# Kernel optimization log

Hardware: AMD Instinct MI355X
Metric: run time of the kernel (lower is better)

Reference implementation:

```python
import jax, jax.numpy as jnp
from jax import lax
import numpy as np

RF = 1024   # receptive field
MGC = 60    # mgc feature size
UPS = 200   # upsample factor
MIX = 10    # num mixtures
FS = 256    # filter size
F = 2       # mgc frames
N = F * UPS
SQRT_HALF = 0.70710678118


def setup_inputs() -> dict:
    key = jax.random.key(0)
    ks = jax.random.split(key, 30)
    g = lambda i, shape, s=0.05: jax.random.normal(ks[i], shape, dtype=jnp.float32) * s
    return dict(
        signal=g(0, (N + RF,), 0.3),
        mgc=g(1, (F, MGC), 1.0),
        cond_w=g(2, (MGC * UPS, MGC)), cond_b=g(3, (MGC * UPS,)),
        l0_win=g(4, (FS, 1, 2)), l0_bin=g(5, (FS,)),
        l0_wg=g(6, (FS, 1, 2)), l0_bg=g(7, (FS,)),
        l0_wr=g(8, (FS, 1, 2)), l0_br=g(9, (FS,)),
        lw_in=g(10, (9, FS, FS, 2)), lb_in=g(11, (9, FS)),
        lw_g=g(12, (9, FS, FS, 2)), lb_g=g(13, (9, FS)),
        lw_r=g(14, (9, FS, FS, 2)), lb_r=g(15, (9, FS)),
        cw_in=g(16, (10, FS, MGC)), cb_in=g(17, (10, FS)),
        cw_g=g(18, (10, FS, MGC)), cb_g=g(19, (10, FS)),
        pre_w=g(20, (256, FS)), pre_b=g(21, (256,)),
        mean_w=g(22, (MIX, 256)), mean_b=g(23, (MIX,)),
        std_w=g(24, (MIX, 256)), std_b=g(25, (MIX,)),
        logit_w=g(26, (MIX, 256)), logit_b=g(27, (MIX,)),
    )


def _cond_conv(x, cond, win, bin_, wg, bg, wr, br, wci, bci, wcg, bcg):
    # x: [N, Cin, L]; cond: [N, MGC] -> out: [N, FS, L//2]
    conv = lambda w, b: lax.conv_general_dilated(
        x, w, window_strides=(2,), padding='VALID',
        dimension_numbers=('NCH', 'OIH', 'NCH')) + b[None, :, None]
    it = jnp.tanh(conv(win, bin_) + (cond @ wci.T + bci)[:, :, None])
    gt = jax.nn.sigmoid(conv(wg, bg) + (cond @ wcg.T + bcg)[:, :, None])
    return (it * gt + conv(wr, br)) * SQRT_HALF


def _forward(signal, mgc, cond_w, cond_b,
             l0_win, l0_bin, l0_wg, l0_bg, l0_wr, l0_br,
             lw_in, lb_in, lw_g, lb_g, lw_r, lb_r,
             cw_in, cb_in, cw_g, cb_g,
             pre_w, pre_b, mean_w, mean_b, std_w, std_b, logit_w, logit_b):
    n = signal.shape[0] - RF
    # sliding windows: [n, 1, RF]
    idx = jnp.arange(n)[:, None] + jnp.arange(RF)[None, :]
    x = signal[idx][:, None, :]
    # conditioning: [F, MGC] -> [F, MGC*UPS] -> [F*UPS, MGC]
    cond = jnp.tanh(mgc @ cond_w.T + cond_b).reshape(-1, MGC)
    # WaveNet stack: 10 stride-2 gated conv layers, L: 1024 -> 1
    x = _cond_conv(x, cond, l0_win, l0_bin, l0_wg, l0_bg, l0_wr, l0_br,
                   cw_in[0], cb_in[0], cw_g[0], cb_g[0])
    for i in range(9):
        x = _cond_conv(x, cond, lw_in[i], lb_in[i], lw_g[i], lb_g[i],
                       lw_r[i], lb_r[i], cw_in[i + 1], cb_in[i + 1],
                       cw_g[i + 1], cb_g[i + 1])
    pre = jax.nn.relu(x[:, :, 0] @ pre_w.T + pre_b)  # [n, 256]
    mean = pre @ mean_w.T + mean_b
    stdev = pre @ std_w.T + std_b
    logits = pre @ logit_w.T + logit_b
    return mean, stdev, logits


def reference(signal, mgc, cond_w, cond_b,
              l0_win, l0_bin, l0_wg, l0_bg, l0_wr, l0_br,
              lw_in, lb_in, lw_g, lb_g, lw_r, lb_r,
              cw_in, cb_in, cw_g, cb_g,
              pre_w, pre_b, mean_w, mean_b, std_w, std_b, logit_w, logit_b):
    return _forward(signal, mgc, cond_w, cond_b,
                    l0_win, l0_bin, l0_wg, l0_bg, l0_wr, l0_br,
                    lw_in, lb_in, lw_g, lb_g, lw_r, lb_r,
                    cw_in, cb_in, cw_g, cb_g,
                    pre_w, pre_b, mean_w, mean_b, std_w, std_b,
                    logit_w, logit_b)
```

## Files before the change

kernel.cpp:

```cpp
#include <hip/hip_runtime.h>

typedef unsigned short u16;
using bf16x8 = __attribute__((ext_vector_type(8))) short;
using f32x4  = __attribute__((ext_vector_type(4))) float;

#define SQRT_HALF 0.70710678118f

__device__ __forceinline__ u16 f2bf(float f) {
    union { float f; unsigned int i; } x; x.f = f;
    unsigned int i = x.i;
    unsigned int r = (i + 0x7FFFu + ((i >> 16) & 1u)) >> 16;
    return (u16)r;
}
__device__ __forceinline__ float bf2f(u16 u) {
    union { unsigned int i; float f; } x; x.i = ((unsigned int)u) << 16; return x.f;
}
__device__ __forceinline__ float fastrcp(float x) {
    float r; asm("v_rcp_f32 %0, %1" : "=v"(r) : "v"(x)); return r;
}
__device__ __forceinline__ float sigm(float x) {
    return fastrcp(1.0f + __expf(-x));
}
__device__ __forceinline__ float tanh_f(float x) {
    float cx = fminf(fmaxf(x, -12.f), 12.f);
    float e = __expf(2.f * cx);
    return 1.0f - 2.0f * fastrcp(e + 1.0f);
}

__device__ __forceinline__ void gld16(const u16* g, u16* l) {
    __builtin_amdgcn_global_load_lds(
        (const __attribute__((address_space(1))) void*)g,
        (__attribute__((address_space(3))) void*)l,
        16, 0, 0);
}

__global__ __launch_bounds__(256) void xpose_kernel(
        const float* __restrict__ cond_w, const float* __restrict__ cw_in,
        const float* __restrict__ cw_g,
        float* __restrict__ cond_wT, float* __restrict__ cwT_in,
        float* __restrict__ cwT_g) {
    int idx = blockIdx.x * 256 + threadIdx.x;
    if (idx < 720000) {
        int c = idx / 12000, j = idx % 12000;
        cond_wT[idx] = cond_w[(size_t)j * 60 + c];
    } else if (idx < 720000 + 153600) {
        int i = idx - 720000;
        int l = i / 15360, r = i % 15360;
        int cc = r / 256, co = r % 256;
        cwT_in[i] = cw_in[((size_t)(l * 256 + co)) * 60 + cc];
    } else if (idx < 720000 + 307200) {
        int i = idx - 720000 - 153600;
        int l = i / 15360, r = i % 15360;
        int cc = r / 256, co = r % 256;
        cwT_g[i] = cw_g[((size_t)(l * 256 + co)) * 60 + cc];
    }
}

__global__ __launch_bounds__(256) void prep_kernel(
        const float* __restrict__ mgc, const float* __restrict__ cond_wT,
        const float* __restrict__ cond_b,
        const float* __restrict__ cwT_in, const float* __restrict__ cb_in,
        const float* __restrict__ cwT_g,  const float* __restrict__ cb_g,
        const float* __restrict__ l0_bin, const float* __restrict__ lb_in,
        const float* __restrict__ l0_bg,  const float* __restrict__ lb_g,
        const float* __restrict__ lw_in, const float* __restrict__ lw_g,
        const float* __restrict__ lw_r,
        float* __restrict__ ca_in, float* __restrict__ ca_g,
        u16* __restrict__ Wg, u16* __restrict__ Wt) {
    int b = blockIdx.x, t = threadIdx.x;
    if (b < 500) {
        __shared__ float c2[8][60];
        int l = b / 50, ng = b % 50;
        int n0 = ng * 8;
        int f = n0 / 200;
        for (int e = t; e < 480; e += 256) {
            int dn = e / 60, cc = e % 60;
            int jj = ((n0 + dn) % 200) * 60 + cc;
            float s = cond_b[jj];
            const float* mrow = mgc + f * 60;
            for (int c = 0; c < 60; ++c) s += mrow[c] * cond_wT[c * 12000 + jj];
            c2[dn][cc] = tanh_f(s);
        }
        __syncthreads();
        int co = t;
        float sib = cb_in[l * 256 + co] + (l == 0 ? l0_bin[co] : lb_in[(l - 1) * 256 + co]);
        float sgb = cb_g [l * 256 + co] + (l == 0 ? l0_bg [co] : lb_g [(l - 1) * 256 + co]);
        float si[8], sg[8];
        #pragma unroll
        for (int dn = 0; dn < 8; ++dn) { si[dn] = sib; sg[dn] = sgb; }
        const float* wiT = cwT_in + l * 15360 + co;
        const float* wgT = cwT_g  + l * 15360 + co;
        for (int cc = 0; cc < 60; ++cc) {
            float wiv = wiT[cc * 256];
            float wgv = wgT[cc * 256];
            #pragma unroll
            for (int dn = 0; dn < 8; ++dn) {
                float cv = c2[dn][cc];
                si[dn] += cv * wiv;
                sg[dn] += cv * wgv;
            }
        }
        #pragma unroll
        for (int dn = 0; dn < 8; ++dn) {
            ca_in[l * 102400 + (n0 + dn) * 256 + co] = si[dn];
            ca_g [l * 102400 + (n0 + dn) * 256 + co] = sg[dn];
        }
    } else if (b < 5108) {
        int idx = (b - 500) * 256 + t;
        if (idx < 9 * 256 * 512) {
            int kk = idx & 511;
            int co = (idx >> 9) & 255;
            int l  = idx >> 17;
            int k = kk >> 8, ci = kk & 255;
            size_t src = ((size_t)(l * 256 + co) * 256 + ci) * 2 + k;
            size_t dst = (size_t)l * 3 * 131072 + (size_t)co * 512 + kk;
            Wg[dst]              = f2bf(lw_in[src]);
            Wg[dst + 131072]     = f2bf(lw_g[src]);
            Wg[dst + 2 * 131072] = f2bf(lw_r[src]);
        }
    } else {
        int c = (b - 5108) * 256 + t;
        if (c < 245760) {
            int lane = c & 63;
            int t1 = c >> 6;
            int cf = t1 & 7;
            int t2 = t1 >> 3;
            int kk = t2 & 15;
            int t3 = t2 >> 4;
            int cb = t3 & 1;
            int t4 = t3 >> 1;
            int cv = t4 % 3;
            int l5 = t4 / 3;
            int q = lane >> 4, r16 = lane & 15;
            int co = cb * 128 + cf * 16 + r16;
            const float* w = cv == 0 ? lw_in : (cv == 1 ? lw_g : lw_r);
            u16* dst = Wt + (size_t)c * 8;
            #pragma unroll
            for (int j = 0; j < 8; ++j) {
                int kdim = kk * 32 + q * 8 + j;
                int tap = kdim >> 8, ci = kdim & 255;
                size_t src = (((size_t)((l5 + 4) * 256 + co)) * 256 + ci) * 2 + tap;
                dst[j] = f2bf(w[src]);
            }
        }
    }
}

__global__ void l0_kernel(const float* __restrict__ signal,
                          const float* __restrict__ l0_win, const float* __restrict__ l0_wg,
                          const float* __restrict__ l0_wr,  const float* __restrict__ l0_br,
                          const float* __restrict__ ca_in0, const float* __restrict__ ca_g0,
                          u16* __restrict__ Y0, int n_start) {
    int b = blockIdx.x;
    int tg = b & 127, n_local = b >> 7;
    int n = n_start + n_local;
    int ci = threadIdx.x;
    float wi0 = l0_win[ci * 2], wi1 = l0_win[ci * 2 + 1];
    float wg0 = l0_wg [ci * 2], wg1 = l0_wg [ci * 2 + 1];
    float wr0 = l0_wr [ci * 2], wr1 = l0_wr [ci * 2 + 1];
    float cain = ca_in0[n * 256 + ci], cag = ca_g0[n * 256 + ci], br = l0_br[ci];
    for (int i = 0; i < 4; ++i) {
        int t = tg * 4 + i;
        float s0 = signal[n + 2 * t];
        float s1 = signal[n + 2 * t + 1];
        float vin = wi0 * s0 + wi1 * s1 + cain;
        float vg  = wg0 * s0 + wg1 * s1 + cag;
        float vr  = wr0 * s0 + wr1 * s1 + br;
        float o = (tanh_f(vin) * sigm(vg) + vr) * SQRT_HALF;
        Y0[((size_t)n_local * 512 + t) * 256 + ci] = f2bf(o);
    }
}

template<int BK>
__global__ __launch_bounds__(256, BK == 32 ? 3 : 2) void gemm_layer_kernel(
        const u16* __restrict__ A, const u16* __restrict__ Wg,
        const float* __restrict__ ca_in, const float* __restrict__ ca_g,
        const float* __restrict__ br, u16* __restrict__ Y,
        int M, int lg, int n_start) {
    constexpr int AC  = BK / 16;
    constexpr int BC  = (3 * BK) / 32;
    constexpr int SL  = BK / 8;
    constexpr int RSH = (BK == 32) ? 2 : 3;
    constexpr int NS  = 512 / BK;

    __shared__ __attribute__((aligned(16))) u16 A0[128 * BK];
    __shared__ __attribute__((aligned(16))) u16 A1[128 * BK];
    __shared__ __attribute__((aligned(16))) u16 B0[192 * BK];
    __shared__ __attribute__((aligned(16))) u16 B1[192 * BK];

    int mtiles = (M + 127) >> 7;
    int b = blockIdx.x;
    int mtile, cotile;
    if ((mtiles & 7) == 0) {
        int g = b >> 5, r = b & 31;
        mtile  = g * 8 + (r & 7);
        cotile = r >> 3;
    } else {
        mtile = b >> 2; cotile = b & 3;
    }
    int m0  = mtile * 128;
    int co0 = cotile * 64;
    int tid = threadIdx.x;
    int lane = tid & 63, wave = tid >> 6;
    int wm = wave & 1, wc = wave >> 1;
    int q = lane >> 4, r16 = lane & 15;

    auto swz = [](int row) { return (BK == 32) ? ((row >> 1) & 3) : (row & 7); };

    const u16* agp[AC]; unsigned aoff[AC];
    #pragma unroll
    for (int i = 0; i < AC; ++i) {
        int c = i * 256 + tid;
        int row = c >> RSH, s = c & (SL - 1);
        int m = m0 + row;
        int msafe = m < M ? m : (M - 1);
        agp[i] = A + (size_t)msafe * 512 + (s ^ swz(row)) * 8;
        aoff[i] = (unsigned)c * 8;
    }
    const u16* bgp[BC]; unsigned boff[BC];
    #pragma unroll
    for (int i = 0; i < BC; ++i) {
        int c = i * 256 + tid;
        int row = c >> RSH, s = c & (SL - 1);
        int conv = row >> 6, col = row & 63;
        bgp[i] = Wg + ((size_t)conv * 256 + co0 + col) * 512 + (s ^ swz(row)) * 8;
        boff[i] = (unsigned)c * 8;
    }

    f32x4 acc[3][4][2] = {};

    auto doIssue = [&](int ktn, u16* Al, u16* Bl) {
        #pragma unroll
        for (int i = 0; i < AC; ++i) gld16(agp[i] + ktn * BK, &Al[aoff[i]]);
        #pragma unroll
        for (int i = 0; i < BC; ++i) gld16(bgp[i] + ktn * BK, &Bl[boff[i]]);
    };
    auto doComp = [&](const u16* Al, const u16* Bl) {
        #pragma unroll
        for (int ks = 0; ks < BK / 32; ++ks) {
            bf16x8 af[4], bfr[3][2];
            #pragma unroll
            for (int ms = 0; ms < 4; ++ms) {
                int row = wm * 64 + ms * 16 + r16;
                af[ms] = *(const bf16x8*)(&Al[row * BK + (((ks * 4 + q) ^ swz(row)) * 8)]);
            }
            #pragma unroll
            for (int cv = 0; cv < 3; ++cv)
                #pragma unroll
                for (int cs = 0; cs < 2; ++cs) {
                    int row = cv * 64 + wc * 32 + cs * 16 + r16;
                    bfr[cv][cs] = *(const bf16x8*)(&Bl[row * BK + (((ks * 4 + q) ^ swz(row)) * 8)]);
                }
            __builtin_amdgcn_s_setprio(1);
            #pragma unroll
            for (int cv = 0; cv < 3; ++cv)
                #pragma unroll
                for (int ms = 0; ms < 4; ++ms)
                    #pragma unroll
                    for (int cs = 0; cs < 2; ++cs)
                        acc[cv][ms][cs] = __builtin_amdgcn_mfma_f32_16x16x32_bf16(
                            af[ms], bfr[cv][cs], acc[cv][ms][cs], 0, 0, 0);
            __builtin_amdgcn_s_setprio(0);
        }
    };
    auto waitv = []() {
        if constexpr (BK == 32)
            asm volatile("s_waitcnt vmcnt(5)\n\ts_barrier" ::: "memory");
        else
            asm volatile("s_waitcnt vmcnt(10)\n\ts_barrier" ::: "memory");
    };

    doIssue(0, A0, B0);
    doIssue(1, A1, B1);
    waitv();

    #pragma unroll
    for (int kt2 = 0; kt2 < NS / 2 - 1; ++kt2) {
        doComp(A0, B0);
        asm volatile("s_waitcnt lgkmcnt(0)\n\ts_barrier" ::: "memory");
        doIssue(2 * kt2 + 2, A0, B0);
        waitv();
        doComp(A1, B1);
        asm volatile("s_waitcnt lgkmcnt(0)\n\ts_barrier" ::: "memory");
        doIssue(2 * kt2 + 3, A1, B1);
        waitv();
    }
    doComp(A0, B0);
    asm volatile("s_waitcnt lgkmcnt(0)\n\ts_barrier" ::: "memory");
    asm volatile("s_waitcnt vmcnt(0)\n\ts_barrier" ::: "memory");
    doComp(A1, B1);

    #pragma unroll
    for (int ms = 0; ms < 4; ++ms) {
        #pragma unroll
        for (int reg = 0; reg < 4; ++reg) {
            int m = m0 + wm * 64 + ms * 16 + q * 4 + reg;
            if (m >= M) continue;
            int n = n_start + (m >> lg);
            #pragma unroll
            for (int cs = 0; cs < 2; ++cs) {
                int co = co0 + wc * 32 + cs * 16 + r16;
                float vin = acc[0][ms][cs][reg] + ca_in[n * 256 + co];
                float vg  = acc[1][ms][cs][reg] + ca_g [n * 256 + co];
                float vr  = acc[2][ms][cs][reg] + br[co];
                float o = (tanh_f(vin) * sigm(vg) + vr) * SQRT_HALF;
                Y[(size_t)m * 256 + co] = f2bf(o);
            }
        }
    }
}

__global__ __launch_bounds__(256, 2) void tail_kernel(
        const u16* __restrict__ Y4, const u16* __restrict__ Wt,
        const float* __restrict__ ca_in, const float* __restrict__ ca_g,
        const float* __restrict__ lb_r,
        const float* __restrict__ pre_w, const float* __restrict__ pre_b,
        const float* __restrict__ mean_w, const float* __restrict__ mean_b,
        const float* __restrict__ std_w,  const float* __restrict__ std_b,
        const float* __restrict__ logit_w, const float* __restrict__ logit_b,
        float* __restrict__ out, int n_start, int n_end) {
    __shared__ __attribute__((aligned(16))) u16 X[2][32][256];
    __shared__ __attribute__((aligned(16))) u16 Yb[2][16][256];
    __shared__ float pre[2][256];

    int tid = threadIdx.x;
    int n0 = n_start + blockIdx.x * 2;

    #pragma unroll
    for (int i = 0; i < 8; ++i) {
        int c = i * 256 + tid;
        int win = c >> 10, rem = c & 1023;
        int row = rem >> 5, blk = rem & 31;
        int n = n0 + win; if (n > n_end - 1) n = n_end - 1;
        const u16* src = Y4 + ((size_t)(n - n_start) * 32 + row) * 256 + blk * 8;
        *(uint4*)(&X[win][row][(blk ^ ((row >> 1) & 7)) * 8]) = *(const uint4*)src;
    }
    __syncthreads();

    int lane = tid & 63, w = tid >> 6;
    int win = w & 1, cobase = (w >> 1) * 128;
    int cb = cobase >> 7;
    int r16 = lane & 15, q = lane >> 4;
    bool wvalid = (n0 + win) < n_end;
    int n = n0 + win;

    for (int l = 5; l <= 9; ++l) {
        int Rout = 512 >> l;
        int Rin  = Rout * 2;
        const u16* IN = (l & 1) ? &X[win][0][0] : &Yb[win][0][0];
        u16*      OUT = (l & 1) ? &Yb[win][0][0] : &X[win][0][0];
        const u16* Wbase = Wt + ((size_t)((l - 5) * 3 * 2 + cb) * 16 * 8) * 512;
        const float* cal  = ca_in + (size_t)l * 102400;
        const float* cagl = ca_g  + (size_t)l * 102400;
        const float* brl  = lb_r + (l - 1) * 256;

        f32x4 acc[3][8] = {};
        #pragma unroll 2
        for (int kk = 0; kk < 16; ++kk) {
            int row = 2 * r16 + (kk >> 3);
            if (row >= Rin) row &= 1;
            bf16x8 af = *(const bf16x8*)(
                &IN[row * 256 + ((((kk & 7) * 4 + q) ^ ((row >> 1) & 7)) * 8)]);
            bf16x8 bfr[3][8];
            #pragma unroll
            for (int cv = 0; cv < 3; ++cv)
                #pragma unroll
                for (int cf = 0; cf < 8; ++cf)
                    bfr[cv][cf] = *(const bf16x8*)(
                        Wbase + ((size_t)(cv * 2 * 16 * 8 + kk * 8 + cf)) * 512 + lane * 8);
            __builtin_amdgcn_s_setprio(1);
            #pragma unroll
            for (int cv = 0; cv < 3; ++cv)
                #pragma unroll
                for (int cf = 0; cf < 8; ++cf)
                    acc[cv][cf] = __builtin_amdgcn_mfma_f32_16x16x32_bf16(
                        af, bfr[cv][cf], acc[cv][cf], 0, 0, 0);
            __builtin_amdgcn_s_setprio(0);
        }

        if (wvalid) {
            #pragma unroll
            for (int cf = 0; cf < 8; ++cf) {
                int co = cobase + cf * 16 + r16;
                #pragma unroll
                for (int reg = 0; reg < 4; ++reg) {
                    int tp = q * 4 + reg;
                    if (tp < Rout) {
                        float vin = acc[0][cf][reg] + cal [n * 256 + co];
                        float vg  = acc[1][cf][reg] + cagl[n * 256 + co];
                        float vr  = acc[2][cf][reg] + brl[co];
                        float o = (tanh_f(vin) * sigm(vg) + vr) * SQRT_HALF;
                        OUT[tp * 256 + (((co >> 3) ^ ((tp >> 1) & 7)) * 8 + (co & 7))] = f2bf(o);
                    }
                }
            }
        }
        __syncthreads();
    }

    {
        int t = tid;
        for (int wn = 0; wn < 2; ++wn) {
            if (n0 + wn >= n_end) break;
            float s = pre_b[t];
            const float* wrow = pre_w + (size_t)t * 256;
            for (int c2 = 0; c2 < 256; ++c2) s += bf2f(Yb[wn][0][c2]) * wrow[c2];
            pre[wn][t] = fmaxf(s, 0.f);
        }
    }
    __syncthreads();
    if (tid < 60) {
        int wn = tid / 30, tt = tid % 30;
        if (n0 + wn < n_end) {
            int head = tt / 10, mix = tt % 10;
            const float* wv = head == 0 ? mean_w : (head == 1 ? std_w : logit_w);
            const float* bb = head == 0 ? mean_b : (head == 1 ? std_b : logit_b);
            float s2 = bb[mix];
            const float* wr = wv + mix * 256;
            for (int c2 = 0; c2 < 256; ++c2) s2 += pre[wn][c2] * wr[c2];
            out[head * 4000 + (n0 + wn) * 10 + mix] = s2;
        }
    }
}

extern "C" void kernel_launch(void* const* d_in, const int* in_sizes, int n_in,
                              void* d_out, int out_size, void* d_ws, size_t ws_size,
                              hipStream_t stream) {
    const float* signal  = (const float*)d_in[0];
    const float* mgc     = (const float*)d_in[1];
    const float* cond_w  = (const float*)d_in[2];
    const float* cond_b  = (const float*)d_in[3];
    const float* l0_win  = (const float*)d_in[4];
    const float* l0_bin  = (const float*)d_in[5];
    const float* l0_wg   = (const float*)d_in[6];
    const float* l0_bg   = (const float*)d_in[7];
    const float* l0_wr   = (const float*)d_in[8];
    const float* l0_br   = (const float*)d_in[9];
    const float* lw_in   = (const float*)d_in[10];
    const float* lb_in   = (const float*)d_in[11];
    const float* lw_g    = (const float*)d_in[12];
    const float* lb_g    = (const float*)d_in[13];
    const float* lw_r    = (const float*)d_in[14];
    const float* lb_r    = (const float*)d_in[15];
    const float* cw_in   = (const float*)d_in[16];
    const float* cb_in   = (const float*)d_in[17];
    const float* cw_g    = (const float*)d_in[18];
    const float* cb_g    = (const float*)d_in[19];
    const float* pre_w   = (const float*)d_in[20];
    const float* pre_b   = (const float*)d_in[21];
    const float* mean_w  = (const float*)d_in[22];
    const float* mean_b  = (const float*)d_in[23];
    const float* std_w   = (const float*)d_in[24];
    const float* std_b   = (const float*)d_in[25];
    const float* logit_w = (const float*)d_in[26];
    const float* logit_b = (const float*)d_in[27];
    float* out = (float*)d_out;

    char* p = (char*)d_ws;
    auto alloc = [&](size_t bytes) -> char* {
        char* r = p; p += (bytes + 255) & ~(size_t)255; return r;
    };
    u16*   Wg      = (u16*)alloc(7077888);
    u16*   Wt      = (u16*)alloc(3932160);
    float* ca_in   = (float*)alloc(4096000);
    float* ca_g    = (float*)alloc(4096000);
    float* cond_wT = (float*)alloc(2880000);
    float* cwT_in  = (float*)alloc(614400);
    float* cwT_g   = (float*)alloc(614400);
    size_t fixedBytes = (size_t)(p - (char*)d_ws);

    int c = 1;
    while (c < 16 && fixedBytes + (104857600ull + 52428800ull) / c + 4096 > ws_size) c <<= 1;
    u16* bufA = (u16*)alloc(104857600ull / c);
    u16* bufB = (u16*)alloc(52428800ull / c);
    int n_count = 400 / c;

    xpose_kernel<<<4013, 256, 0, stream>>>(cond_w, cw_in, cw_g, cond_wT, cwT_in, cwT_g);
    prep_kernel<<<6068, 256, 0, stream>>>(mgc, cond_wT, cond_b,
                                          cwT_in, cb_in, cwT_g, cb_g,
                                          l0_bin, lb_in, l0_bg, lb_g,
                                          lw_in, lw_g, lw_r, ca_in, ca_g, Wg, Wt);

    for (int ch = 0; ch < c; ++ch) {
        int n_start = ch * n_count;
        l0_kernel<<<n_count * 128, 256, 0, stream>>>(signal, l0_win, l0_wg, l0_wr, l0_br,
                                                     ca_in, ca_g, bufA, n_start);
        u16* src = bufA;
        u16* dst = bufB;
        for (int layer = 1; layer <= 4; ++layer) {
            int lg = 9 - layer;
            int M = n_count << lg;
            int mtiles = (M + 127) / 128;
            if (layer == 2)
                gemm_layer_kernel<64><<<mtiles * 4, 256, 0, stream>>>(
                    src, Wg + (size_t)(layer - 1) * 3 * 131072,
                    ca_in + (size_t)layer * 102400, ca_g + (size_t)layer * 102400,
                    lb_r + (layer - 1) * 256, dst, M, lg, n_start);
            else
                gemm_layer_kernel<32><<<mtiles * 4, 256, 0, stream>>>(
                    src, Wg + (size_t)(layer - 1) * 3 * 131072,
                    ca_in + (size_t)layer * 102400, ca_g + (size_t)layer * 102400,
                    lb_r + (layer - 1) * 256, dst, M, lg, n_start);
            u16* tswap = src; src = dst; dst = tswap;
        }
        int nblk = (n_count + 1) / 2;
        tail_kernel<<<nblk, 256, 0, stream>>>(src, Wt, ca_in, ca_g, lb_r,
                                              pre_w, pre_b, mean_w, mean_b,
                                              std_w, std_b, logit_w, logit_b,
                                              out, n_start, n_start + n_count);
    }
}
```

Measured before the change: 493.0 us.

## Share weight fragments across both windows per wave and double-buffer B loads

Each wave now computes half of a 128-channel output slice for both windows in the block, rather than one window across the full slice. Every loaded weight fragment therefore feeds two MFMAs, which halves per-wave global weight traffic relative to MFMA work. B-fragment loads are also double-buffered across k-steps so they overlap with the MFMAs. The cost is more live accumulators and prefetch registers, which may reduce occupancy, and both windows' epilogues now run in every wave.

New measurement: 484.5 us. Within noise of the previous version (-1.7%).

```diff
diff --git a/kernel.cpp b/kernel.cpp
--- a/kernel.cpp
+++ b/kernel.cpp
@@ -338,59 +338,84 @@
     __syncthreads();
 
     int lane = tid & 63, w = tid >> 6;
-    int win = w & 1, cobase = (w >> 1) * 128;
-    int cb = cobase >> 7;
+    int cb = w >> 1, cfh = (w & 1) * 4;
     int r16 = lane & 15, q = lane >> 4;
-    bool wvalid = (n0 + win) < n_end;
-    int n = n0 + win;
+    bool v1 = (n0 + 1) < n_end;
 
     for (int l = 5; l <= 9; ++l) {
         int Rout = 512 >> l;
         int Rin  = Rout * 2;
-        const u16* IN = (l & 1) ? &X[win][0][0] : &Yb[win][0][0];
-        u16*      OUT = (l & 1) ? &Yb[win][0][0] : &X[win][0][0];
+        const u16* IN0 = (l & 1) ? &X[0][0][0] : &Yb[0][0][0];
+        const u16* IN1 = (l & 1) ? &X[1][0][0] : &Yb[1][0][0];
+        u16* OUT0 = (l & 1) ? &Yb[0][0][0] : &X[0][0][0];
+        u16* OUT1 = (l & 1) ? &Yb[1][0][0] : &X[1][0][0];
         const u16* Wbase = Wt + ((size_t)((l - 5) * 3 * 2 + cb) * 16 * 8) * 512;
         const float* cal  = ca_in + (size_t)l * 102400;
         const float* cagl = ca_g  + (size_t)l * 102400;
         const float* brl  = lb_r + (l - 1) * 256;
 
-        f32x4 acc[3][8] = {};
-        #pragma unroll 2
-        for (int kk = 0; kk < 16; ++kk) {
+        f32x4 acc[3][4][2] = {};
+
+        auto loadB = [&](int kk, bf16x8* dst) {
+            #pragma unroll
+            for (int cv = 0; cv < 3; ++cv)
+                #pragma unroll
+                for (int cf = 0; cf < 4; ++cf)
+                    dst[cv * 4 + cf] = *(const bf16x8*)(
+                        Wbase + ((size_t)(cv * 2 * 16 * 8 + kk * 8 + cfh + cf)) * 512 + lane * 8);
+        };
+        auto loadA = [&](int kk, const u16* IN) -> bf16x8 {
             int row = 2 * r16 + (kk >> 3);
             if (row >= Rin) row &= 1;
-            bf16x8 af = *(const bf16x8*)(
+            return *(const bf16x8*)(
                 &IN[row * 256 + ((((kk & 7) * 4 + q) ^ ((row >> 1) & 7)) * 8)]);
-            bf16x8 bfr[3][8];
+        };
+        auto doMfma = [&](const bf16x8* bw, int kk) {
+            bf16x8 a0 = loadA(kk, IN0);
+            bf16x8 a1 = loadA(kk, IN1);
+            __builtin_amdgcn_s_setprio(1);
             #pragma unroll
             for (int cv = 0; cv < 3; ++cv)
                 #pragma unroll
-                for (int cf = 0; cf < 8; ++cf)
-                    bfr[cv][cf] = *(const bf16x8*)(
-                        Wbase + ((size_t)(cv * 2 * 16 * 8 + kk * 8 + cf)) * 512 + lane * 8);
-            __builtin_amdgcn_s_setprio(1);
-            #pragma unroll
-            for (int cv = 0; cv < 3; ++cv)
-                #pragma unroll
-                for (int cf = 0; cf < 8; ++cf)
-                    acc[cv][cf] = __builtin_amdgcn_mfma_f32_16x16x32_bf16(
-                        af, bfr[cv][cf], acc[cv][cf], 0, 0, 0);
+                for (int cf = 0; cf < 4; ++cf) {
+                    acc[cv][cf][0] = __builtin_amdgcn_mfma_f32_16x16x32_bf16(
+                        a0, bw[cv * 4 + cf], acc[cv][cf][0], 0, 0, 0);
+                    acc[cv][cf][1] = __builtin_amdgcn_mfma_f32_16x16x32_bf16(
+                        a1, bw[cv * 4 + cf], acc[cv][cf][1], 0, 0, 0);
+                }
             __builtin_amdgcn_s_setprio(0);
-        }
-
-        if (wvalid) {
-            #pragma unroll
-            for (int cf = 0; cf < 8; ++cf) {
-                int co = cobase + cf * 16 + r16;
-                #pragma unroll
-                for (int reg = 0; reg < 4; ++reg) {
-                    int tp = q * 4 + reg;
-                    if (tp < Rout) {
-                        float vin = acc[0][cf][reg] + cal [n * 256 + co];
-                        float vg  = acc[1][cf][reg] + cagl[n * 256 + co];
-                        float vr  = acc[2][cf][reg] + brl[co];
+        };
+
+        bf16x8 bA[12], bB[12];
+        loadB(0, bA);
+        #pragma unroll
+        for (int kp = 0; kp < 16; kp += 2) {
+            loadB(kp + 1, bB);
+            doMfma(bA, kp);
+            if (kp + 2 < 16) loadB(kp + 2, bA);
+            doMfma(bB, kp + 1);
+        }
+
+        #pragma unroll
+        for (int cf = 0; cf < 4; ++cf) {
+            int co = (cb * 2 + (cfh >> 2)) * 64 + cf * 16 + r16;
+            #pragma unroll
+            for (int reg = 0; reg < 4; ++reg) {
+                int tp = q * 4 + reg;
+                if (tp < Rout) {
+                    {
+                        float vin = acc[0][cf][0][reg] + cal [n0 * 256 + co];
+                        float vg  = acc[1][cf][0][reg] + cagl[n0 * 256 + co];
+                        float vr  = acc[2][cf][0][reg] + brl[co];
                         float o = (tanh_f(vin) * sigm(vg) + vr) * SQRT_HALF;
-                        OUT[tp * 256 + (((co >> 3) ^ ((tp >> 1) & 7)) * 8 + (co & 7))] = f2bf(o);
+                        OUT0[tp * 256 + (((co >> 3) ^ ((tp >> 1) & 7)) * 8 + (co & 7))] = f2bf(o);
+                    }
+                    if (v1) {
+                        float vin = acc[0][cf][1][reg] + cal [(n0 + 1) * 256 + co];
+                        float vg  = acc[1][cf][1][reg] + cagl[(n0 + 1) * 256 + co];
+                        float vr  = acc[2][cf][1][reg] + brl[co];
+                        float o = (tanh_f(vin) * sigm(vg) + vr) * SQRT_HALF;
+                        OUT1[tp * 256 + (((co >> 3) ^ ((tp >> 1) & 7)) * 8 + (co & 7))] = f2bf(o);
                     }
                 }
             }
```
